# Kernel tuning notes

Measured on AMD Instinct MI355X. Metric: run time of the kernel, lower is better.

## Reference

```python
import jax, jax.numpy as jnp
import numpy as np

B, C, H, W = 16, 256, 64, 64
K, HID, ITERS, EPS = 4, 512, 3, 1e-8


def _ln(x, g, b, eps=1e-5):
    m = jnp.mean(x, axis=-1, keepdims=True)
    v = jnp.mean((x - m) ** 2, axis=-1, keepdims=True)
    return (x - m) * jax.lax.rsqrt(v + eps) * g + b


def setup_inputs() -> dict:
    key = jax.random.key(0)
    ks = jax.random.split(key, 24)

    def lin(k, o, i):
        lim = np.sqrt(6.0 / (o + i)).astype(np.float32)
        return jax.random.uniform(k, (o, i), jnp.float32, -lim, lim)

    return {
        "x": jax.random.normal(ks[0], (B, C, H, W), jnp.float32),
        "noise": jax.random.normal(ks[1], (B, K, C), jnp.float32),
        "slot_mu": jax.random.normal(ks[2], (1, 1, C), jnp.float32),
        "slot_log_sigma": jnp.zeros((1, 1, C), jnp.float32),
        "ln_in_g": jnp.ones((C,)), "ln_in_b": jnp.zeros((C,)),
        "ln_sl_g": jnp.ones((C,)), "ln_sl_b": jnp.zeros((C,)),
        "ln_mlp_g": jnp.ones((C,)), "ln_mlp_b": jnp.zeros((C,)),
        "Wq": lin(ks[3], C, C), "bq": jnp.zeros((C,)),
        "Wk": lin(ks[4], C, C), "bk": jnp.zeros((C,)),
        "Wv": lin(ks[5], C, C), "bv": jnp.zeros((C,)),
        "Wu": lin(ks[6], C, 2 * C), "bu": jnp.zeros((C,)),
        "W1": lin(ks[7], HID, C), "b1": jnp.zeros((HID,)),
        "W2": lin(ks[8], C, HID), "b2": jnp.zeros((C,)),
        "We1": lin(ks[9], C // 2, C), "be1": jnp.zeros((C // 2,)),
        "We2": lin(ks[10], 1, C // 2), "be2": jnp.zeros((1,)),
    }


def reference(x, noise, slot_mu, slot_log_sigma, ln_in_g, ln_in_b, ln_sl_g, ln_sl_b,
              ln_mlp_g, ln_mlp_b, Wq, bq, Wk, bk, Wv, bv, Wu, bu, W1, b1, W2, b2,
              We1, be1, We2, be2):
    # b c h w -> b (h w) c
    xn = x.reshape(B, C, H * W).transpose(0, 2, 1)
    xn = _ln(xn, ln_in_g, ln_in_b)
    # k, v depend only on xn; hoisted out of the loop (same math)
    k = jnp.einsum('bnc,dc->bnd', xn, Wk) + bk
    v = jnp.einsum('bnc,dc->bnd', xn, Wv) + bv
    scale = C ** (-0.5)
    slots = slot_mu + jnp.exp(slot_log_sigma) * noise
    for _ in range(ITERS):
        prev = slots
        s = _ln(slots, ln_sl_g, ln_sl_b)
        q = jnp.einsum('bkc,dc->bkd', s, Wq) + bq
        attn = jax.nn.softmax(jnp.einsum('bkc,bnc->bkn', q, k) * scale, axis=1)
        w = attn / (jnp.sum(attn, axis=-1, keepdims=True) + EPS)
        updates = jnp.einsum('bkn,bnc->bkc', w, v)
        combined = jnp.concatenate([prev, updates], axis=-1)  # (B,K,2C)
        slots = jnp.einsum('bkc,dc->bkd', combined, Wu) + bu + prev
        m = _ln(slots, ln_mlp_g, ln_mlp_b)
        h = jax.nn.gelu(jnp.einsum('bkc,hc->bkh', m, W1) + b1, approximate=False)
        slots = slots + jnp.einsum('bkh,ch->bkc', h, W2) + b2
    e = jax.nn.gelu(jnp.einsum('bkc,dc->bkd', slots, We1) + be1, approximate=False)
    slot_weights = jax.nn.sigmoid(jnp.einsum('bkd,od->bko', e, We2) + be2)[..., 0]
    return slots, slot_weights
```

## Files before the change

kernel.cpp:

```cpp
#include <hip/hip_runtime.h>
#include <math.h>

#define B_    16
#define C_    256
#define NPIX  4096
#define K_    4
#define HID_  512
#define ITERS_ 3
#define NROWS (B_*NPIX)
#define EPS_  1e-8f

typedef __attribute__((ext_vector_type(8))) short bf16x8;
typedef __attribute__((ext_vector_type(4))) float f32x4;

__device__ __forceinline__ float gelu_f(float x) {
    return 0.5f * x * (1.0f + erff(x * 0.70710678118654752f));
}

__device__ __forceinline__ unsigned short f2bf(float x) {
    union { float f; unsigned u; } v; v.f = x;
    unsigned r = v.u + 0x7fffu + ((v.u >> 16) & 1u);
    return (unsigned short)(r >> 16);
}
__device__ __forceinline__ float bflo(unsigned u) {
    union { unsigned u; float f; } v; v.u = u << 16; return v.f;
}
__device__ __forceinline__ float bfhi(unsigned u) {
    union { unsigned u; float f; } v; v.u = u & 0xffff0000u; return v.f;
}
__device__ __forceinline__ float4 shfl_xor4(float4 v, int m) {
    v.x = __shfl_xor(v.x, m); v.y = __shfl_xor(v.y, m);
    v.z = __shfl_xor(v.z, m); v.w = __shfl_xor(v.w, m);
    return v;
}
__device__ __forceinline__ void fma4(float4& a, const float4 w, const float4 s) {
    a.x = fmaf(w.x, s.x, a.x); a.y = fmaf(w.y, s.y, a.y);
    a.z = fmaf(w.z, s.z, a.z); a.w = fmaf(w.w, s.w, a.w);
}
__device__ __forceinline__ float hsum4(const float4 a) {
    return (a.x + a.y) + (a.z + a.w);
}

__device__ __forceinline__ void reduce256_in1024(float* red1, float* red2, int tid,
                                                 float& o1, float& o2) {
    __syncthreads();
    for (int s = 128; s > 0; s >>= 1) {
        if (tid < s) { red1[tid] += red1[tid + s]; red2[tid] += red2[tid + s]; }
        __syncthreads();
    }
    o1 = red1[0]; o2 = red2[0];
    __syncthreads();
}

__global__ void prep_kernel(const float* __restrict__ Wq, const float* __restrict__ Wu,
                            const float* __restrict__ W1, const float* __restrict__ W2,
                            const float* __restrict__ We1, const float* __restrict__ Wk,
                            const float* __restrict__ Wv,
                            float4* __restrict__ Wq4, float4* __restrict__ Wu4,
                            float4* __restrict__ W14, float4* __restrict__ W24,
                            float4* __restrict__ We14, float4* __restrict__ Wkq4,
                            float4* __restrict__ Wv4) {
    int i = blockIdx.x * 256 + threadIdx.x;
    if (i < 16384) {
        int c4 = i >> 8, d = i & 255;
        Wq4[i] = *(const float4*)&Wq[d * 256 + c4 * 4];
    } else if (i < 49152) {
        int j = i - 16384; int c4 = j >> 8, d = j & 255;
        Wu4[j] = *(const float4*)&Wu[d * 512 + c4 * 4];
    } else if (i < 81920) {
        int j = i - 49152; int c4 = j >> 9, h = j & 511;
        W14[j] = *(const float4*)&W1[h * 256 + c4 * 4];
    } else if (i < 114688) {
        int j = i - 81920; int h4 = j >> 8, d = j & 255;
        W24[j] = *(const float4*)&W2[d * 512 + h4 * 4];
    } else if (i < 122880) {
        int j = i - 114688; int c4 = j >> 7, e = j & 127;
        We14[j] = *(const float4*)&We1[e * 256 + c4 * 4];
    } else if (i < 139264) {
        int j = i - 122880; int d4 = j >> 8, c = j & 255;
        float4 o;
        o.x = Wk[(4 * d4 + 0) * 256 + c];
        o.y = Wk[(4 * d4 + 1) * 256 + c];
        o.z = Wk[(4 * d4 + 2) * 256 + c];
        o.w = Wk[(4 * d4 + 3) * 256 + c];
        Wkq4[j] = o;
    } else {
        int j = i - 139264; int e4 = j >> 8, d = j & 255;
        Wv4[j] = *(const float4*)&Wv[d * 256 + e4 * 4];
    }
}

__global__ __launch_bounds__(256) void xn_fused_kernel(
    const float* __restrict__ x, const float* __restrict__ g, const float* __restrict__ bta,
    unsigned short* __restrict__ xnb) {
    __shared__ float tile[256][65];
    __shared__ float sg[256], sb[256];
    __shared__ float red1[256], red2[256];
    __shared__ float smean[64], srstd[64];
    const int tid = threadIdx.x;
    const int nt = blockIdx.x << 6, b = blockIdx.y;

    sg[tid] = g[tid]; sb[tid] = bta[tid];
    #pragma unroll
    for (int r = 0; r < 64; ++r) {
        int idx = tid + (r << 8);
        int c_l = idx >> 6, n_l = idx & 63;
        tile[c_l][n_l] = x[(size_t)(b * C_ + c_l) * NPIX + nt + n_l];
    }
    __syncthreads();
    {
        int cq = tid >> 6, n_l = tid & 63;
        float s = 0.f, s2 = 0.f;
        #pragma unroll 8
        for (int c = cq * 64; c < cq * 64 + 64; ++c) {
            float v = tile[c][n_l];
            s += v; s2 += v * v;
        }
        red1[tid] = s; red2[tid] = s2;
    }
    __syncthreads();
    if (tid < 64) {
        float s  = red1[tid] + red1[tid + 64] + red1[tid + 128] + red1[tid + 192];
        float s2 = red2[tid] + red2[tid + 64] + red2[tid + 128] + red2[tid + 192];
        float m = s * (1.0f / C_);
        smean[tid] = m;
        srstd[tid] = rsqrtf(s2 * (1.0f / C_) - m * m + 1e-5f);
    }
    __syncthreads();
    #pragma unroll
    for (int r = 0; r < 32; ++r) {
        int idx = tid + (r << 8);
        int n_l = idx >> 7, cp = idx & 127;
        int c0 = cp << 1;
        float mn = smean[n_l], rs = srstd[n_l];
        float v0 = (tile[c0][n_l] - mn) * rs * sg[c0] + sb[c0];
        float v1 = (tile[c0 + 1][n_l] - mn) * rs * sg[c0 + 1] + sb[c0 + 1];
        ushort2 o; o.x = f2bf(v0); o.y = f2bf(v1);
        *reinterpret_cast<ushort2*>(&xnb[((size_t)(b * NPIX + nt + n_l)) * C_ + c0]) = o;
    }
}


__device__ __forceinline__ void ln_q_qt_1024(
    float v, int tid, int d, int q, int r,
    const float* __restrict__ g_sl, const float* __restrict__ b_sl,
    const float4* __restrict__ Wq4, const float* __restrict__ bq,
    const float4* __restrict__ Wkq4, const float* __restrict__ bk,
    float* __restrict__ qtbuf, float* __restrict__ qoffbuf,
    float* snorm, float* qrow, float* pq, float* redA, float* redB) {
    if (q == 0) { redA[d] = v; redB[d] = v * v; }
    float sm, s2;
    reduce256_in1024(redA, redB, tid, sm, s2);
    if (q == 0) {
        float m = sm * (1.f / C_);
        float rs = rsqrtf(s2 * (1.f / C_) - m * m + 1e-5f);
        snorm[d] = (v - m) * rs * g_sl[d] + b_sl[d];
    }
    __syncthreads();
    {
        const float4* sn4 = (const float4*)snorm;
        float4 a0 = {0,0,0,0}, a1 = {0,0,0,0};
        int c4b = q << 4;
        #pragma unroll
        for (int i = 0; i < 16; i += 2) {
            fma4(a0, Wq4[(c4b + i) * 256 + d], sn4[c4b + i]);
            fma4(a1, Wq4[(c4b + i + 1) * 256 + d], sn4[c4b + i + 1]);
        }
        pq[q * 256 + d] = hsum4(a0) + hsum4(a1);
    }
    __syncthreads();
    if (q == 0) {
        float qfull = pq[d] + pq[256 + d] + pq[512 + d] + pq[768 + d] + bq[d];
        qrow[d] = qfull;
        redA[d] = qfull * bk[d]; redB[d] = 0.f;
    }
    float qoffv, dummy;
    reduce256_in1024(redA, redB, tid, qoffv, dummy);
    if (tid == 0) qoffbuf[r] = qoffv;
    {
        const float4* q4 = (const float4*)qrow;
        float4 a0 = {0,0,0,0}, a1 = {0,0,0,0};
        int d4b = q << 4;
        #pragma unroll
        for (int i = 0; i < 16; i += 2) {
            fma4(a0, Wkq4[(d4b + i) * 256 + d], q4[d4b + i]);
            fma4(a1, Wkq4[(d4b + i + 1) * 256 + d], q4[d4b + i + 1]);
        }
        pq[q * 256 + d] = hsum4(a0) + hsum4(a1);
    }
    __syncthreads();
    if (q == 0)
        qtbuf[r * C_ + d] = pq[d] + pq[256 + d] + pq[512 + d] + pq[768 + d];
}

__global__ __launch_bounds__(1024) void slot_init_q_kernel(
    const float* __restrict__ noise, const float* __restrict__ mu,
    const float* __restrict__ log_sigma,
    const float* __restrict__ g_sl, const float* __restrict__ b_sl,
    const float4* __restrict__ Wq4, const float* __restrict__ bq,
    const float4* __restrict__ Wkq4, const float* __restrict__ bk,
    float* __restrict__ slots, float* __restrict__ qtbuf, float* __restrict__ qoffbuf,
    float* __restrict__ usum, float* __restrict__ denom) {
    __shared__ __align__(16) float snorm[256];
    __shared__ __align__(16) float qrow[256];
    __shared__ float pq[1024];
    __shared__ float redA[256], redB[256];
    int tid = threadIdx.x;
    int d = tid & 255, q = tid >> 8;
    int r = blockIdx.x;
    float v = 0.f;
    if (q == 0) {
        v = mu[d] + expf(log_sigma[d]) * noise[r * C_ + d];
        slots[r * C_ + d] = v;
        usum[r * C_ + d] = 0.f;
    }
    if (tid == 0) denom[r] = 0.f;
    ln_q_qt_1024(v, tid, d, q, r, g_sl, b_sl, Wq4, bq, Wkq4, bk,
                 qtbuf, qoffbuf, snorm, qrow, pq, redA, redB);
}

__device__ __forceinline__ float slot_update_body(
    int tid, int d, int q, int r, const float* __restrict__ slots,
    float* __restrict__ usum, float* __restrict__ denom,
    const float4* __restrict__ Wv4, const float* __restrict__ bv,
    const float4* __restrict__ Wu4, const float* __restrict__ bu,
    const float* __restrict__ g_mlp, const float* __restrict__ b_mlp,
    const float4* __restrict__ W14, const float* __restrict__ b1,
    const float4* __restrict__ W24, const float* __restrict__ b2,
    float* comb, float* pq, float* mrow, float* hrow,
    float* redA, float* redB, float* s_denom, float* s_scale) {
    float uv = 0.f;
    if (q == 0) {
        uv = usum[r * C_ + d];
        usum[r * C_ + d] = 0.f;
    }
    if (tid == 0) {
        float dv = denom[r];
        *s_denom = dv + EPS_;
        *s_scale = dv / (dv + EPS_);
        denom[r] = 0.f;
    }
    float prev = 0.f;
    if (q == 0) prev = slots[r * C_ + d];
    __syncthreads();
    if (q == 0) {
        comb[d] = prev;
        mrow[d] = uv / *s_denom;
    }
    __syncthreads();
    {
        const float4* u4 = (const float4*)mrow;
        float4 a0 = {0,0,0,0}, a1 = {0,0,0,0};
        int e4b = q << 4;
        #pragma unroll
        for (int i = 0; i < 16; i += 2) {
            fma4(a0, Wv4[(e4b + i) * 256 + d], u4[e4b + i]);
            fma4(a1, Wv4[(e4b + i + 1) * 256 + d], u4[e4b + i + 1]);
        }
        pq[q * 256 + d] = hsum4(a0) + hsum4(a1);
    }
    __syncthreads();
    if (q == 0)
        comb[256 + d] = pq[d] + pq[256 + d] + pq[512 + d] + pq[768 + d] + *s_scale * bv[d];
    __syncthreads();
    const float4* cb4 = (const float4*)comb;
    {
        float4 a0 = {0,0,0,0}, a1 = {0,0,0,0}, a2 = {0,0,0,0}, a3 = {0,0,0,0};
        int c4b = q << 5;
        #pragma unroll
        for (int i = 0; i < 32; i += 4) {
            float4 w0 = Wu4[(c4b + i + 0) * 256 + d];
            float4 w1 = Wu4[(c4b + i + 1) * 256 + d];
            float4 w2 = Wu4[(c4b + i + 2) * 256 + d];
            float4 w3 = Wu4[(c4b + i + 3) * 256 + d];
            fma4(a0, w0, cb4[c4b + i + 0]); fma4(a1, w1, cb4[c4b + i + 1]);
            fma4(a2, w2, cb4[c4b + i + 2]); fma4(a3, w3, cb4[c4b + i + 3]);
        }
        pq[q * 256 + d] = (hsum4(a0) + hsum4(a1)) + (hsum4(a2) + hsum4(a3));
    }
    __syncthreads();
    float nv = 0.f;
    if (q == 0) {
        nv = pq[d] + pq[256 + d] + pq[512 + d] + pq[768 + d] + bu[d] + prev;
        redA[d] = nv; redB[d] = nv * nv;
    }
    float sm, s2;
    reduce256_in1024(redA, redB, tid, sm, s2);
    if (q == 0) {
        float m = sm * (1.f / C_);
        float rs = rsqrtf(s2 * (1.f / C_) - m * m + 1e-5f);
        mrow[d] = (nv - m) * rs * g_mlp[d] + b_mlp[d];
    }
    __syncthreads();
    const float4* m4 = (const float4*)mrow;
    {
        int j = tid & 511, h2 = tid >> 9;
        float4 a0 = {0,0,0,0}, a1 = {0,0,0,0};
        int c4b = h2 << 5;
        #pragma unroll
        for (int i = 0; i < 32; i += 2) {
            float4 w0 = W14[(c4b + i + 0) * 512 + j];
            float4 w1 = W14[(c4b + i + 1) * 512 + j];
            fma4(a0, w0, m4[c4b + i + 0]); fma4(a1, w1, m4[c4b + i + 1]);
        }
        pq[h2 * 512 + j] = hsum4(a0) + hsum4(a1);
    }
    __syncthreads();
    if (tid < 512) hrow[tid] = gelu_f(pq[tid] + pq[512 + tid] + b1[tid]);
    __syncthreads();
    const float4* h4 = (const float4*)hrow;
    {
        float4 a0 = {0,0,0,0}, a1 = {0,0,0,0}, a2 = {0,0,0,0}, a3 = {0,0,0,0};
        int h4b = q << 5;
        #pragma unroll
        for (int i = 0; i < 32; i += 4) {
            float4 w0 = W24[(h4b + i + 0) * 256 + d];
            float4 w1 = W24[(h4b + i + 1) * 256 + d];
            float4 w2 = W24[(h4b + i + 2) * 256 + d];
            float4 w3 = W24[(h4b + i + 3) * 256 + d];
            fma4(a0, w0, h4[h4b + i + 0]); fma4(a1, w1, h4[h4b + i + 1]);
            fma4(a2, w2, h4[h4b + i + 2]); fma4(a3, w3, h4[h4b + i + 3]);
        }
        pq[q * 256 + d] = (hsum4(a0) + hsum4(a1)) + (hsum4(a2) + hsum4(a3));
    }
    __syncthreads();
    float ov = 0.f;
    if (q == 0)
        ov = nv + pq[d] + pq[256 + d] + pq[512 + d] + pq[768 + d] + b2[d];
    return ov;
}

__global__ __launch_bounds__(1024) void slot_update_q_kernel(
    float* __restrict__ slots, float* __restrict__ usum, float* __restrict__ denom,
    const float4* __restrict__ Wv4, const float* __restrict__ bv,
    const float4* __restrict__ Wu4, const float* __restrict__ bu,
    const float* __restrict__ g_mlp, const float* __restrict__ b_mlp,
    const float4* __restrict__ W14, const float* __restrict__ b1,
    const float4* __restrict__ W24, const float* __restrict__ b2,
    const float* __restrict__ g_sl, const float* __restrict__ b_sl,
    const float4* __restrict__ Wq4, const float* __restrict__ bq,
    const float4* __restrict__ Wkq4, const float* __restrict__ bk,
    float* __restrict__ qtbuf, float* __restrict__ qoffbuf) {
    __shared__ __align__(16) float comb[512];
    __shared__ __align__(16) float mrow[256];
    __shared__ __align__(16) float hrow[512];
    __shared__ float pq[1024];
    __shared__ float redA[256], redB[256];
    __shared__ float s_denom, s_scale;
    int tid = threadIdx.x;
    int d = tid & 255, q = tid >> 8;
    int r = blockIdx.x;
    float ov = slot_update_body(tid, d, q, r, slots, usum, denom, Wv4, bv, Wu4, bu,
                                g_mlp, b_mlp, W14, b1, W24, b2,
                                comb, pq, mrow, hrow, redA, redB, &s_denom, &s_scale);
    if (q == 0) slots[r * C_ + d] = ov;
    __syncthreads();
    ln_q_qt_1024(ov, tid, d, q, r, g_sl, b_sl, Wq4, bq, Wkq4, bk,
                 qtbuf, qoffbuf, mrow, comb, pq, redA, redB);
}

__global__ __launch_bounds__(1024) void slot_update_final_kernel(
    float* __restrict__ slots, float* __restrict__ usum, float* __restrict__ denom,
    const float4* __restrict__ Wv4, const float* __restrict__ bv,
    const float4* __restrict__ Wu4, const float* __restrict__ bu,
    const float* __restrict__ g_mlp, const float* __restrict__ b_mlp,
    const float4* __restrict__ W14, const float* __restrict__ b1,
    const float4* __restrict__ W24, const float* __restrict__ b2,
    const float4* __restrict__ We14, const float* __restrict__ be1,
    const float* __restrict__ We2, const float* __restrict__ be2,
    float* __restrict__ out) {
    __shared__ __align__(16) float comb[512];
    __shared__ __align__(16) float mrow[256];
    __shared__ __align__(16) float hrow[512];
    __shared__ float pq[1024];
    __shared__ float redA[256], redB[256];
    __shared__ float s_denom, s_scale;
    __shared__ float erow[128];
    int tid = threadIdx.x;
    int d = tid & 255, q = tid >> 8;
    int r = blockIdx.x;
    float ov = slot_update_body(tid, d, q, r, slots, usum, denom, Wv4, bv, Wu4, bu,
                                g_mlp, b_mlp, W14, b1, W24, b2,
                                comb, pq, mrow, hrow, redA, redB, &s_denom, &s_scale);
    if (q == 0) {
        out[r * C_ + d] = ov;
        mrow[d] = ov;
    }
    __syncthreads();
    const float4* m4 = (const float4*)mrow;
    {
        int e = tid & 127, o8 = tid >> 7;
        float4 a0 = {0,0,0,0}, a1 = {0,0,0,0};
        int c4b = o8 << 3;
        #pragma unroll
        for (int i = 0; i < 8; i += 2) {
            fma4(a0, We14[(c4b + i) * 128 + e], m4[c4b + i]);
            fma4(a1, We14[(c4b + i + 1) * 128 + e], m4[c4b + i + 1]);
        }
        pq[o8 * 128 + e] = hsum4(a0) + hsum4(a1);
    }
    __syncthreads();
    if (tid < 128) {
        float s = 0.f;
        #pragma unroll
        for (int o = 0; o < 8; ++o) s += pq[o * 128 + tid];
        erow[tid] = gelu_f(s + be1[tid]);
    }
    __syncthreads();
    if (tid < 64) {
        float p = We2[tid] * erow[tid] + We2[tid + 64] * erow[tid + 64];
        #pragma unroll
        for (int m = 1; m <= 32; m <<= 1) p += __shfl_xor(p, m);
        if (tid == 0) out[B_ * K_ * C_ + r] = 1.0f / (1.0f + expf(-(p + be2[0])));
    }
}

__global__ __launch_bounds__(256) void attn_fused_kernel(
    const float* __restrict__ qtbuf, const float* __restrict__ qoffbuf,
    const unsigned short* __restrict__ xnb,
    float* __restrict__ usum, float* __restrict__ denom) {
    __shared__ float4 qT[264];
    __shared__ float attns[K_][64];
    __shared__ float upd_s[K_][256];
    __shared__ float asw[4][4];
    __shared__ float4 qo_s;

    const int tid = threadIdx.x;
    const int b = blockIdx.y;
    const int chunk = blockIdx.x;
    const int n0 = chunk << 6;
    const int wave = tid >> 6, lane = tid & 63;

    {
        int c = tid;
        float4 qv;
        qv.x = qtbuf[b * 1024 + c];
        qv.y = qtbuf[b * 1024 + 256 + c];
        qv.z = qtbuf[b * 1024 + 512 + c];
        qv.w = qtbuf[b * 1024 + 768 + c];
        qT[c + (c >> 5)] = qv;
        if (tid == 0) qo_s = *(const float4*)&qoffbuf[b * 4];
    }
    __syncthreads();

    const int cpart = tid & 7;
    const int npair = tid >> 3;
    const int c0 = cpart << 5;
    float4 acc0 = {0.f, 0.f, 0.f, 0.f}, acc1 = {0.f, 0.f, 0.f, 0.f};
    const unsigned short* kbase = xnb + ((size_t)b * NPIX + n0 + npair * 2) * C_ + c0;
    #pragma unroll
    for (int j = 0; j < 4; ++j) {
        uint4 k0 = *reinterpret_cast<const uint4*>(kbase + j * 8);
        uint4 k1 = *reinterpret_cast<const uint4*>(kbase + C_ + j * 8);
        const unsigned kw0[4] = {k0.x, k0.y, k0.z, k0.w};
        const unsigned kw1[4] = {k1.x, k1.y, k1.z, k1.w};
        #pragma unroll
        for (int jj = 0; jj < 4; ++jj) {
            int cidx = c0 + j * 8 + jj * 2 + cpart;
            float4 qa = qT[cidx];
            float4 qb = qT[cidx + 1];
            float f00 = bflo(kw0[jj]), f01 = bfhi(kw0[jj]);
            float f10 = bflo(kw1[jj]), f11 = bfhi(kw1[jj]);
            acc0.x += f00 * qa.x + f01 * qb.x;  acc0.y += f00 * qa.y + f01 * qb.y;
            acc0.z += f00 * qa.z + f01 * qb.z;  acc0.w += f00 * qa.w + f01 * qb.w;
            acc1.x += f10 * qa.x + f11 * qb.x;  acc1.y += f10 * qa.y + f11 * qb.y;
            acc1.z += f10 * qa.z + f11 * qb.z;  acc1.w += f10 * qa.w + f11 * qb.w;
        }
    }
    #pragma unroll
    for (int m = 1; m <= 4; m <<= 1) {
        acc0 = acc0 + shfl_xor4(acc0, m);
        acc1 = acc1 + shfl_xor4(acc1, m);
    }
    float4 w0, w1;
    {
        float4 l = (acc0 + qo_s) * 0.0625f;
        float mx = fmaxf(fmaxf(l.x, l.y), fmaxf(l.z, l.w));
        w0.x = expf(l.x - mx); w0.y = expf(l.y - mx);
        w0.z = expf(l.z - mx); w0.w = expf(l.w - mx);
        float inv = 1.0f / (w0.x + w0.y + w0.z + w0.w);
        w0 = w0 * inv;
        l = (acc1 + qo_s) * 0.0625f;
        mx = fmaxf(fmaxf(l.x, l.y), fmaxf(l.z, l.w));
        w1.x = expf(l.x - mx); w1.y = expf(l.y - mx);
        w1.z = expf(l.z - mx); w1.w = expf(l.w - mx);
        inv = 1.0f / (w1.x + w1.y + w1.z + w1.w);
        w1 = w1 * inv;
    }
    if (cpart == 0) {
        int n_l = npair * 2;
        attns[0][n_l] = w0.x; attns[1][n_l] = w0.y; attns[2][n_l] = w0.z; attns[3][n_l] = w0.w;
        attns[0][n_l + 1] = w1.x; attns[1][n_l + 1] = w1.y;
        attns[2][n_l + 1] = w1.z; attns[3][n_l + 1] = w1.w;
    }
    float4 ws = w0 + w1;
    #pragma unroll
    for (int m = 8; m <= 32; m <<= 1) ws = ws + shfl_xor4(ws, m);
    if (lane == 0) {
        asw[wave][0] = ws.x; asw[wave][1] = ws.y; asw[wave][2] = ws.z; asw[wave][3] = ws.w;
    }
    __syncthreads();
    if (tid < 4)
        atomicAdd(&denom[b * 4 + tid],
                  asw[0][tid] + asw[1][tid] + asw[2][tid] + asw[3][tid]);

    const int h = wave >> 1;
    const int chalf = (wave & 1) << 7;
    const int c = chalf + lane * 2;
    float a0[K_] = {0.f, 0.f, 0.f, 0.f};
    float a1[K_] = {0.f, 0.f, 0.f, 0.f};
    const unsigned short* vbase = xnb + ((size_t)b * NPIX + n0 + h * 32) * C_ + c;
    #pragma unroll 4
    for (int nn = 0; nn < 32; ++nn) {
        unsigned vv = *reinterpret_cast<const unsigned*>(vbase + (size_t)nn * C_);
        float v0 = bflo(vv), v1 = bfhi(vv);
        int n_l = h * 32 + nn;
        float q0 = attns[0][n_l], q1 = attns[1][n_l], q2 = attns[2][n_l], q3 = attns[3][n_l];
        a0[0] = fmaf(q0, v0, a0[0]); a1[0] = fmaf(q0, v1, a1[0]);
        a0[1] = fmaf(q1, v0, a0[1]); a1[1] = fmaf(q1, v1, a1[1]);
        a0[2] = fmaf(q2, v0, a0[2]); a1[2] = fmaf(q2, v1, a1[2]);
        a0[3] = fmaf(q3, v0, a0[3]); a1[3] = fmaf(q3, v1, a1[3]);
    }
    __syncthreads();
    if (h == 0) {
        #pragma unroll
        for (int k = 0; k < K_; ++k) { upd_s[k][c] = a0[k]; upd_s[k][c + 1] = a1[k]; }
    }
    __syncthreads();
    if (h == 1) {
        #pragma unroll
        for (int k = 0; k < K_; ++k) { upd_s[k][c] += a0[k]; upd_s[k][c + 1] += a1[k]; }
    }
    __syncthreads();
    #pragma unroll
    for (int k = 0; k < K_; ++k)
        atomicAdd(&usum[((size_t)b * K_ + k) * 256 + tid], upd_s[k][tid]);
}

extern "C" void kernel_launch(void* const* d_in, const int* in_sizes, int n_in,
                              void* d_out, int out_size, void* d_ws, size_t ws_size,
                              hipStream_t stream) {
    (void)in_sizes; (void)n_in; (void)out_size; (void)ws_size;
    const float* x        = (const float*)d_in[0];
    const float* noise    = (const float*)d_in[1];
    const float* slot_mu  = (const float*)d_in[2];
    const float* slot_ls  = (const float*)d_in[3];
    const float* ln_in_g  = (const float*)d_in[4];
    const float* ln_in_b  = (const float*)d_in[5];
    const float* ln_sl_g  = (const float*)d_in[6];
    const float* ln_sl_b  = (const float*)d_in[7];
    const float* ln_mlp_g = (const float*)d_in[8];
    const float* ln_mlp_b = (const float*)d_in[9];
    const float* Wq = (const float*)d_in[10];
    const float* bq = (const float*)d_in[11];
    const float* Wk = (const float*)d_in[12];
    const float* bk = (const float*)d_in[13];
    const float* Wv = (const float*)d_in[14];
    const float* bv = (const float*)d_in[15];
    const float* Wu = (const float*)d_in[16];
    const float* bu = (const float*)d_in[17];
    const float* W1 = (const float*)d_in[18];
    const float* b1 = (const float*)d_in[19];
    const float* W2 = (const float*)d_in[20];
    const float* b2 = (const float*)d_in[21];
    const float* We1 = (const float*)d_in[22];
    const float* be1 = (const float*)d_in[23];
    const float* We2 = (const float*)d_in[24];
    const float* be2 = (const float*)d_in[25];
    float* out = (float*)d_out;

    char* ws = (char*)d_ws;
    unsigned short* xnb = (unsigned short*)ws;
    float4* Wq4  = (float4*)(xnb + (size_t)NROWS * C_);
    float4* Wu4  = Wq4 + 16384;
    float4* W14  = Wu4 + 32768;
    float4* W24  = W14 + 32768;
    float4* We14 = W24 + 32768;
    float4* Wkq4 = We14 + 8192;
    float4* Wv4  = Wkq4 + 16384;
    float* slots = (float*)(Wv4 + 16384);
    float* qtbuf = slots + B_ * K_ * C_;
    float* qoffb = qtbuf + B_ * K_ * C_;
    float* usum  = qoffb + B_ * K_;
    float* denom = usum + B_ * K_ * C_;

    prep_kernel<<<608, 256, 0, stream>>>(Wq, Wu, W1, W2, We1, Wk, Wv,
                                         Wq4, Wu4, W14, W24, We14, Wkq4, Wv4);
    xn_fused_kernel<<<dim3(64, 16), 256, 0, stream>>>(x, ln_in_g, ln_in_b, xnb);
    slot_init_q_kernel<<<B_ * K_, 1024, 0, stream>>>(noise, slot_mu, slot_ls,
                                                     ln_sl_g, ln_sl_b, Wq4, bq, Wkq4, bk,
                                                     slots, qtbuf, qoffb, usum, denom);
    for (int it = 0; it < ITERS_; ++it) {
        attn_fused_kernel<<<dim3(64, 16), 256, 0, stream>>>(qtbuf, qoffb, xnb,
                                                            usum, denom);
        if (it < ITERS_ - 1) {
            slot_update_q_kernel<<<B_ * K_, 1024, 0, stream>>>(
                slots, usum, denom, Wv4, bv, Wu4, bu, ln_mlp_g, ln_mlp_b,
                W14, b1, W24, b2, ln_sl_g, ln_sl_b, Wq4, bq, Wkq4, bk, qtbuf, qoffb);
        } else {
            slot_update_final_kernel<<<B_ * K_, 1024, 0, stream>>>(
                slots, usum, denom, Wv4, bv, Wu4, bu, ln_mlp_g, ln_mlp_b,
                W14, b1, W24, b2, We14, be1, We2, be2, out);
        }
    }
}
```

Measured before the change: 321.9 us.

## Precompose Wu·Wv and Wk^T·Wq weights, use wave-shuffle reductions in slot kernels

```diff
diff --git a/kernel.cpp b/kernel.cpp
--- a/kernel.cpp
+++ b/kernel.cpp
@@ -10,9 +10,6 @@
 #define NROWS (B_*NPIX)
 #define EPS_  1e-8f
 
-typedef __attribute__((ext_vector_type(8))) short bf16x8;
-typedef __attribute__((ext_vector_type(4))) float f32x4;
-
 __device__ __forceinline__ float gelu_f(float x) {
     return 0.5f * x * (1.0f + erff(x * 0.70710678118654752f));
 }
@@ -41,52 +38,91 @@
     return (a.x + a.y) + (a.z + a.w);
 }
 
-__device__ __forceinline__ void reduce256_in1024(float* red1, float* red2, int tid,
-                                                 float& o1, float& o2) {
-    __syncthreads();
-    for (int s = 128; s > 0; s >>= 1) {
-        if (tid < s) { red1[tid] += red1[tid + s]; red2[tid] += red2[tid + s]; }
+__device__ __forceinline__ void redpair256(float a, float b, int tid, int q,
+                                           float* r8, float& o1, float& o2) {
+    if (q == 0) {
+        #pragma unroll
+        for (int m = 1; m <= 32; m <<= 1) { a += __shfl_xor(a, m); b += __shfl_xor(b, m); }
+        if ((tid & 63) == 0) { r8[(tid >> 6) * 2] = a; r8[(tid >> 6) * 2 + 1] = b; }
+    }
+    __syncthreads();
+    o1 = r8[0] + r8[2] + r8[4] + r8[6];
+    o2 = r8[1] + r8[3] + r8[5] + r8[7];
+    __syncthreads();
+}
+
+__global__ __launch_bounds__(256) void prep_pack_kernel(
+    const float* __restrict__ Wu, const float* __restrict__ W1,
+    const float* __restrict__ W2, const float* __restrict__ We1,
+    const float* __restrict__ Wq, const float* __restrict__ bk,
+    const float* __restrict__ bq,
+    float4* __restrict__ WuC4, float4* __restrict__ W14,
+    float4* __restrict__ W24, float4* __restrict__ We14,
+    float* __restrict__ wqoff) {
+    __shared__ float r4[4];
+    int i = blockIdx.x * 256 + threadIdx.x;
+    if (blockIdx.x == 352) {
+        int c = threadIdx.x;
+        float s = 0.f;
+        for (int dd = 0; dd < 256; ++dd) s = fmaf(Wq[dd * 256 + c], bk[dd], s);
+        wqoff[c] = s;
+        float p = bq[c] * bk[c];
+        #pragma unroll
+        for (int m = 1; m <= 32; m <<= 1) p += __shfl_xor(p, m);
+        if ((c & 63) == 0) r4[c >> 6] = p;
         __syncthreads();
-    }
-    o1 = red1[0]; o2 = red2[0];
-    __syncthreads();
-}
-
-__global__ void prep_kernel(const float* __restrict__ Wq, const float* __restrict__ Wu,
-                            const float* __restrict__ W1, const float* __restrict__ W2,
-                            const float* __restrict__ We1, const float* __restrict__ Wk,
-                            const float* __restrict__ Wv,
-                            float4* __restrict__ Wq4, float4* __restrict__ Wu4,
-                            float4* __restrict__ W14, float4* __restrict__ W24,
-                            float4* __restrict__ We14, float4* __restrict__ Wkq4,
-                            float4* __restrict__ Wv4) {
-    int i = blockIdx.x * 256 + threadIdx.x;
+        if (c == 0) wqoff[256] = r4[0] + r4[1] + r4[2] + r4[3];
+        return;
+    }
     if (i < 16384) {
-        int c4 = i >> 8, d = i & 255;
-        Wq4[i] = *(const float4*)&Wq[d * 256 + c4 * 4];
+        int c4 = i >> 8, dd = i & 255;
+        WuC4[i] = *(const float4*)&Wu[dd * 512 + c4 * 4];
     } else if (i < 49152) {
-        int j = i - 16384; int c4 = j >> 8, d = j & 255;
-        Wu4[j] = *(const float4*)&Wu[d * 512 + c4 * 4];
+        int j = i - 16384; int c4 = j >> 9, h = j & 511;
+        W14[j] = *(const float4*)&W1[h * 256 + c4 * 4];
     } else if (i < 81920) {
-        int j = i - 49152; int c4 = j >> 9, h = j & 511;
-        W14[j] = *(const float4*)&W1[h * 256 + c4 * 4];
-    } else if (i < 114688) {
-        int j = i - 81920; int h4 = j >> 8, d = j & 255;
-        W24[j] = *(const float4*)&W2[d * 512 + h4 * 4];
-    } else if (i < 122880) {
-        int j = i - 114688; int c4 = j >> 7, e = j & 127;
+        int j = i - 49152; int h4 = j >> 8, dd = j & 255;
+        W24[j] = *(const float4*)&W2[dd * 512 + h4 * 4];
+    } else {
+        int j = i - 81920; int c4 = j >> 7, e = j & 127;
         We14[j] = *(const float4*)&We1[e * 256 + c4 * 4];
-    } else if (i < 139264) {
-        int j = i - 122880; int d4 = j >> 8, c = j & 255;
-        float4 o;
-        o.x = Wk[(4 * d4 + 0) * 256 + c];
-        o.y = Wk[(4 * d4 + 1) * 256 + c];
-        o.z = Wk[(4 * d4 + 2) * 256 + c];
-        o.w = Wk[(4 * d4 + 3) * 256 + c];
-        Wkq4[j] = o;
-    } else {
-        int j = i - 139264; int e4 = j >> 8, d = j & 255;
-        Wv4[j] = *(const float4*)&Wv[d * 256 + e4 * 4];
+    }
+}
+
+__global__ __launch_bounds__(256) void prep_compose_kernel(
+    const float* __restrict__ Wu, const float* __restrict__ Wv,
+    const float* __restrict__ Wk, const float* __restrict__ Wq,
+    const float* __restrict__ bv, const float* __restrict__ bq,
+    float4* __restrict__ WuC4, float4* __restrict__ Wqk4,
+    float* __restrict__ bv2, float* __restrict__ bqk) {
+    __shared__ float wur[256], wkc[256];
+    __shared__ float ldsA[256], ldsB[256];
+    __shared__ float r1[4], r2[4];
+    const int d = blockIdx.x, c = threadIdx.x;
+    wur[c] = Wu[d * 512 + 256 + c];
+    wkc[c] = Wk[c * 256 + d];
+    __syncthreads();
+    float a = 0.f, b = 0.f;
+    #pragma unroll 4
+    for (int e = 0; e < 256; ++e) {
+        a = fmaf(wur[e], Wv[e * 256 + c], a);
+        b = fmaf(wkc[e], Wq[e * 256 + c], b);
+    }
+    ldsA[c] = a; ldsB[c] = b;
+    float p1 = wur[c] * bv[c], p2 = wkc[c] * bq[c];
+    #pragma unroll
+    for (int m = 1; m <= 32; m <<= 1) { p1 += __shfl_xor(p1, m); p2 += __shfl_xor(p2, m); }
+    if ((c & 63) == 0) { r1[c >> 6] = p1; r2[c >> 6] = p2; }
+    __syncthreads();
+    if (c < 64) {
+        float4 qa = { ldsA[4 * c], ldsA[4 * c + 1], ldsA[4 * c + 2], ldsA[4 * c + 3] };
+        float4 qb = { ldsB[4 * c], ldsB[4 * c + 1], ldsB[4 * c + 2], ldsB[4 * c + 3] };
+        WuC4[(64 + c) * 256 + d] = qa;
+        Wqk4[c * 256 + d] = qb;
+    }
+    if (c == 0) {
+        bv2[d] = r1[0] + r1[1] + r1[2] + r1[3];
+        bqk[d] = r2[0] + r2[1] + r2[2] + r2[3];
     }
 }
 
@@ -141,16 +177,16 @@
 }
 
 
-__device__ __forceinline__ void ln_q_qt_1024(
+__device__ __forceinline__ void ln_qt_1024(
     float v, int tid, int d, int q, int r,
     const float* __restrict__ g_sl, const float* __restrict__ b_sl,
-    const float4* __restrict__ Wq4, const float* __restrict__ bq,
-    const float4* __restrict__ Wkq4, const float* __restrict__ bk,
+    const float4* __restrict__ Wqk4, const float* __restrict__ bqk,
+    const float* __restrict__ wqoff,
     float* __restrict__ qtbuf, float* __restrict__ qoffbuf,
-    float* snorm, float* qrow, float* pq, float* redA, float* redB) {
-    if (q == 0) { redA[d] = v; redB[d] = v * v; }
+    float* snorm, float* pq, float* r8) {
+    float a = (q == 0) ? v : 0.f;
     float sm, s2;
-    reduce256_in1024(redA, redB, tid, sm, s2);
+    redpair256(a, a * v, tid, q, r8, sm, s2);
     if (q == 0) {
         float m = sm * (1.f / C_);
         float rs = rsqrtf(s2 * (1.f / C_) - m * m + 1e-5f);
@@ -163,48 +199,30 @@
         int c4b = q << 4;
         #pragma unroll
         for (int i = 0; i < 16; i += 2) {
-            fma4(a0, Wq4[(c4b + i) * 256 + d], sn4[c4b + i]);
-            fma4(a1, Wq4[(c4b + i + 1) * 256 + d], sn4[c4b + i + 1]);
+            fma4(a0, Wqk4[(c4b + i) * 256 + d], sn4[c4b + i]);
+            fma4(a1, Wqk4[(c4b + i + 1) * 256 + d], sn4[c4b + i + 1]);
         }
         pq[q * 256 + d] = hsum4(a0) + hsum4(a1);
     }
-    __syncthreads();
-    if (q == 0) {
-        float qfull = pq[d] + pq[256 + d] + pq[512 + d] + pq[768 + d] + bq[d];
-        qrow[d] = qfull;
-        redA[d] = qfull * bk[d]; redB[d] = 0.f;
-    }
-    float qoffv, dummy;
-    reduce256_in1024(redA, redB, tid, qoffv, dummy);
-    if (tid == 0) qoffbuf[r] = qoffv;
-    {
-        const float4* q4 = (const float4*)qrow;
-        float4 a0 = {0,0,0,0}, a1 = {0,0,0,0};
-        int d4b = q << 4;
-        #pragma unroll
-        for (int i = 0; i < 16; i += 2) {
-            fma4(a0, Wkq4[(d4b + i) * 256 + d], q4[d4b + i]);
-            fma4(a1, Wkq4[(d4b + i + 1) * 256 + d], q4[d4b + i + 1]);
-        }
-        pq[q * 256 + d] = hsum4(a0) + hsum4(a1);
-    }
-    __syncthreads();
+    float p = (q == 0) ? snorm[d] * wqoff[d] : 0.f;
+    float qo, dum;
+    redpair256(p, 0.f, tid, q, r8, qo, dum);
+    if (tid == 0) qoffbuf[r] = qo + wqoff[256];
     if (q == 0)
-        qtbuf[r * C_ + d] = pq[d] + pq[256 + d] + pq[512 + d] + pq[768 + d];
+        qtbuf[r * C_ + d] = pq[d] + pq[256 + d] + pq[512 + d] + pq[768 + d] + bqk[d];
 }
 
 __global__ __launch_bounds__(1024) void slot_init_q_kernel(
     const float* __restrict__ noise, const float* __restrict__ mu,
     const float* __restrict__ log_sigma,
     const float* __restrict__ g_sl, const float* __restrict__ b_sl,
-    const float4* __restrict__ Wq4, const float* __restrict__ bq,
-    const float4* __restrict__ Wkq4, const float* __restrict__ bk,
+    const float4* __restrict__ Wqk4, const float* __restrict__ bqk,
+    const float* __restrict__ wqoff,
     float* __restrict__ slots, float* __restrict__ qtbuf, float* __restrict__ qoffbuf,
     float* __restrict__ usum, float* __restrict__ denom) {
     __shared__ __align__(16) float snorm[256];
-    __shared__ __align__(16) float qrow[256];
     __shared__ float pq[1024];
-    __shared__ float redA[256], redB[256];
+    __shared__ float r8[8];
     int tid = threadIdx.x;
     int d = tid & 255, q = tid >> 8;
     int r = blockIdx.x;
@@ -215,24 +233,25 @@
         usum[r * C_ + d] = 0.f;
     }
     if (tid == 0) denom[r] = 0.f;
-    ln_q_qt_1024(v, tid, d, q, r, g_sl, b_sl, Wq4, bq, Wkq4, bk,
-                 qtbuf, qoffbuf, snorm, qrow, pq, redA, redB);
+    ln_qt_1024(v, tid, d, q, r, g_sl, b_sl, Wqk4, bqk, wqoff,
+               qtbuf, qoffbuf, snorm, pq, r8);
 }
 
 __device__ __forceinline__ float slot_update_body(
     int tid, int d, int q, int r, const float* __restrict__ slots,
     float* __restrict__ usum, float* __restrict__ denom,
-    const float4* __restrict__ Wv4, const float* __restrict__ bv,
-    const float4* __restrict__ Wu4, const float* __restrict__ bu,
+    const float* __restrict__ bv2,
+    const float4* __restrict__ WuC4, const float* __restrict__ bu,
     const float* __restrict__ g_mlp, const float* __restrict__ b_mlp,
     const float4* __restrict__ W14, const float* __restrict__ b1,
     const float4* __restrict__ W24, const float* __restrict__ b2,
     float* comb, float* pq, float* mrow, float* hrow,
-    float* redA, float* redB, float* s_denom, float* s_scale) {
-    float uv = 0.f;
+    float* r8, float* s_denom, float* s_scale) {
+    float uv = 0.f, prev = 0.f;
     if (q == 0) {
         uv = usum[r * C_ + d];
         usum[r * C_ + d] = 0.f;
+        prev = slots[r * C_ + d];
     }
     if (tid == 0) {
         float dv = denom[r];
@@ -240,28 +259,11 @@
         *s_scale = dv / (dv + EPS_);
         denom[r] = 0.f;
     }
-    float prev = 0.f;
-    if (q == 0) prev = slots[r * C_ + d];
     __syncthreads();
     if (q == 0) {
         comb[d] = prev;
-        mrow[d] = uv / *s_denom;
-    }
-    __syncthreads();
-    {
-        const float4* u4 = (const float4*)mrow;
-        float4 a0 = {0,0,0,0}, a1 = {0,0,0,0};
-        int e4b = q << 4;
-        #pragma unroll
-        for (int i = 0; i < 16; i += 2) {
-            fma4(a0, Wv4[(e4b + i) * 256 + d], u4[e4b + i]);
-            fma4(a1, Wv4[(e4b + i + 1) * 256 + d], u4[e4b + i + 1]);
-        }
-        pq[q * 256 + d] = hsum4(a0) + hsum4(a1);
-    }
-    __syncthreads();
-    if (q == 0)
-        comb[256 + d] = pq[d] + pq[256 + d] + pq[512 + d] + pq[768 + d] + *s_scale * bv[d];
+        comb[256 + d] = uv / *s_denom;
+    }
     __syncthreads();
     const float4* cb4 = (const float4*)comb;
     {
@@ -269,23 +271,24 @@
         int c4b = q << 5;
         #pragma unroll
         for (int i = 0; i < 32; i += 4) {
-            float4 w0 = Wu4[(c4b + i + 0) * 256 + d];
-            float4 w1 = Wu4[(c4b + i + 1) * 256 + d];
-            float4 w2 = Wu4[(c4b + i + 2) * 256 + d];
-            float4 w3 = Wu4[(c4b + i + 3) * 256 + d];
+            float4 w0 = WuC4[(c4b + i + 0) * 256 + d];
+            float4 w1 = WuC4[(c4b + i + 1) * 256 + d];
+            float4 w2 = WuC4[(c4b + i + 2) * 256 + d];
+            float4 w3 = WuC4[(c4b + i + 3) * 256 + d];
             fma4(a0, w0, cb4[c4b + i + 0]); fma4(a1, w1, cb4[c4b + i + 1]);
             fma4(a2, w2, cb4[c4b + i + 2]); fma4(a3, w3, cb4[c4b + i + 3]);
         }
         pq[q * 256 + d] = (hsum4(a0) + hsum4(a1)) + (hsum4(a2) + hsum4(a3));
     }
     __syncthreads();
-    float nv = 0.f;
-    if (q == 0) {
-        nv = pq[d] + pq[256 + d] + pq[512 + d] + pq[768 + d] + bu[d] + prev;
-        redA[d] = nv; redB[d] = nv * nv;
+    float nv = 0.f, aa = 0.f;
+    if (q == 0) {
+        nv = pq[d] + pq[256 + d] + pq[512 + d] + pq[768 + d]
+           + bu[d] + prev + (*s_scale) * bv2[d];
+        aa = nv;
     }
     float sm, s2;
-    reduce256_in1024(redA, redB, tid, sm, s2);
+    redpair256(aa, aa * nv, tid, q, r8, sm, s2);
     if (q == 0) {
         float m = sm * (1.f / C_);
         float rs = rsqrtf(s2 * (1.f / C_) - m * m + 1e-5f);
@@ -332,37 +335,36 @@
 
 __global__ __launch_bounds__(1024) void slot_update_q_kernel(
     float* __restrict__ slots, float* __restrict__ usum, float* __restrict__ denom,
-    const float4* __restrict__ Wv4, const float* __restrict__ bv,
-    const float4* __restrict__ Wu4, const float* __restrict__ bu,
+    const float* __restrict__ bv2,
+    const float4* __restrict__ WuC4, const float* __restrict__ bu,
     const float* __restrict__ g_mlp, const float* __restrict__ b_mlp,
     const float4* __restrict__ W14, const float* __restrict__ b1,
     const float4* __restrict__ W24, const float* __restrict__ b2,
     const float* __restrict__ g_sl, const float* __restrict__ b_sl,
-    const float4* __restrict__ Wq4, const float* __restrict__ bq,
-    const float4* __restrict__ Wkq4, const float* __restrict__ bk,
+    const float4* __restrict__ Wqk4, const float* __restrict__ bqk,
+    const float* __restrict__ wqoff,
     float* __restrict__ qtbuf, float* __restrict__ qoffbuf) {
     __shared__ __align__(16) float comb[512];
     __shared__ __align__(16) float mrow[256];
     __shared__ __align__(16) float hrow[512];
     __shared__ float pq[1024];
-    __shared__ float redA[256], redB[256];
+    __shared__ float r8[8];
     __shared__ float s_denom, s_scale;
     int tid = threadIdx.x;
     int d = tid & 255, q = tid >> 8;
     int r = blockIdx.x;
-    float ov = slot_update_body(tid, d, q, r, slots, usum, denom, Wv4, bv, Wu4, bu,
+    float ov = slot_update_body(tid, d, q, r, slots, usum, denom, bv2, WuC4, bu,
                                 g_mlp, b_mlp, W14, b1, W24, b2,
-                                comb, pq, mrow, hrow, redA, redB, &s_denom, &s_scale);
+                                comb, pq, mrow, hrow, r8, &s_denom, &s_scale);
     if (q == 0) slots[r * C_ + d] = ov;
-    __syncthreads();
-    ln_q_qt_1024(ov, tid, d, q, r, g_sl, b_sl, Wq4, bq, Wkq4, bk,
-                 qtbuf, qoffbuf, mrow, comb, pq, redA, redB);
+    ln_qt_1024(ov, tid, d, q, r, g_sl, b_sl, Wqk4, bqk, wqoff,
+               qtbuf, qoffbuf, mrow, pq, r8);
 }
 
 __global__ __launch_bounds__(1024) void slot_update_final_kernel(
     float* __restrict__ slots, float* __restrict__ usum, float* __restrict__ denom,
-    const float4* __restrict__ Wv4, const float* __restrict__ bv,
-    const float4* __restrict__ Wu4, const float* __restrict__ bu,
+    const float* __restrict__ bv2,
+    const float4* __restrict__ WuC4, const float* __restrict__ bu,
     const float* __restrict__ g_mlp, const float* __restrict__ b_mlp,
     const float4* __restrict__ W14, const float* __restrict__ b1,
     const float4* __restrict__ W24, const float* __restrict__ b2,
@@ -373,15 +375,15 @@
     __shared__ __align__(16) float mrow[256];
     __shared__ __align__(16) float hrow[512];
     __shared__ float pq[1024];
-    __shared__ float redA[256], redB[256];
+    __shared__ float r8[8];
     __shared__ float s_denom, s_scale;
     __shared__ float erow[128];
     int tid = threadIdx.x;
     int d = tid & 255, q = tid >> 8;
     int r = blockIdx.x;
-    float ov = slot_update_body(tid, d, q, r, slots, usum, denom, Wv4, bv, Wu4, bu,
+    float ov = slot_update_body(tid, d, q, r, slots, usum, denom, bv2, WuC4, bu,
                                 g_mlp, b_mlp, W14, b1, W24, b2,
-                                comb, pq, mrow, hrow, redA, redB, &s_denom, &s_scale);
+                                comb, pq, mrow, hrow, r8, &s_denom, &s_scale);
     if (q == 0) {
         out[r * C_ + d] = ov;
         mrow[d] = ov;
@@ -571,35 +573,38 @@
 
     char* ws = (char*)d_ws;
     unsigned short* xnb = (unsigned short*)ws;
-    float4* Wq4  = (float4*)(xnb + (size_t)NROWS * C_);
-    float4* Wu4  = Wq4 + 16384;
-    float4* W14  = Wu4 + 32768;
+    float4* WuC4 = (float4*)(xnb + (size_t)NROWS * C_);
+    float4* W14  = WuC4 + 32768;
     float4* W24  = W14 + 32768;
     float4* We14 = W24 + 32768;
-    float4* Wkq4 = We14 + 8192;
-    float4* Wv4  = Wkq4 + 16384;
-    float* slots = (float*)(Wv4 + 16384);
+    float4* Wqk4 = We14 + 8192;
+    float* bv2   = (float*)(Wqk4 + 16384);
+    float* bqk   = bv2 + 256;
+    float* wqoff = bqk + 256;
+    float* slots = wqoff + 260;
     float* qtbuf = slots + B_ * K_ * C_;
     float* qoffb = qtbuf + B_ * K_ * C_;
     float* usum  = qoffb + B_ * K_;
     float* denom = usum + B_ * K_ * C_;
 
-    prep_kernel<<<608, 256, 0, stream>>>(Wq, Wu, W1, W2, We1, Wk, Wv,
-                                         Wq4, Wu4, W14, W24, We14, Wkq4, Wv4);
+    prep_pack_kernel<<<353, 256, 0, stream>>>(Wu, W1, W2, We1, Wq, bk, bq,
+                                              WuC4, W14, W24, We14, wqoff);
+    prep_compose_kernel<<<256, 256, 0, stream>>>(Wu, Wv, Wk, Wq, bv, bq,
+                                                 WuC4, Wqk4, bv2, bqk);
     xn_fused_kernel<<<dim3(64, 16), 256, 0, stream>>>(x, ln_in_g, ln_in_b, xnb);
     slot_init_q_kernel<<<B_ * K_, 1024, 0, stream>>>(noise, slot_mu, slot_ls,
-                                                     ln_sl_g, ln_sl_b, Wq4, bq, Wkq4, bk,
+                                                     ln_sl_g, ln_sl_b, Wqk4, bqk, wqoff,
                                                      slots, qtbuf, qoffb, usum, denom);
     for (int it = 0; it < ITERS_; ++it) {
         attn_fused_kernel<<<dim3(64, 16), 256, 0, stream>>>(qtbuf, qoffb, xnb,
                                                             usum, denom);
         if (it < ITERS_ - 1) {
             slot_update_q_kernel<<<B_ * K_, 1024, 0, stream>>>(
-                slots, usum, denom, Wv4, bv, Wu4, bu, ln_mlp_g, ln_mlp_b,
-                W14, b1, W24, b2, ln_sl_g, ln_sl_b, Wq4, bq, Wkq4, bk, qtbuf, qoffb);
+                slots, usum, denom, bv2, WuC4, bu, ln_mlp_g, ln_mlp_b,
+                W14, b1, W24, b2, ln_sl_g, ln_sl_b, Wqk4, bqk, wqoff, qtbuf, qoffb);
         } else {
             slot_update_final_kernel<<<B_ * K_, 1024, 0, stream>>>(
-                slots, usum, denom, Wv4, bv, Wu4, bu, ln_mlp_g, ln_mlp_b,
+                slots, usum, denom, bv2, WuC4, bu, ln_mlp_g, ln_mlp_b,
                 W14, b1, W24, b2, We14, be1, We2, be2, out);
         }
     }
```

New measurement: 307.0 us. -4.6%, faster.
